# Performance work log

Hardware: AMD Instinct MI355X
Metric: run time of the kernel (lower is better)

## Reference

```python
import jax, jax.numpy as jnp
import numpy as np

N, E, D, HID, OUT, R = 100000, 640000, 128, 128, 128, 8


def setup_inputs() -> dict:
    key = jax.random.key(0)
    ks = jax.random.split(key, 12)
    x = jax.random.normal(ks[0], (N, D), dtype=jnp.float32)
    src = jax.random.randint(ks[1], (E,), 0, N)
    dst = jax.random.randint(ks[2], (E,), 0, N)
    etype = jax.random.randint(ks[3], (E,), 0, R)
    s = 0.05
    W_rel = jax.random.normal(ks[4], (R, D, OUT), dtype=jnp.float32) * s
    loop_w = jax.random.normal(ks[5], (D, OUT), dtype=jnp.float32) * s
    rel_bias = jax.random.normal(ks[6], (OUT,), dtype=jnp.float32) * s
    W1 = jax.random.normal(ks[7], (D + HID, 2 * HID), dtype=jnp.float32) * s
    b1 = jax.random.normal(ks[8], (2 * HID,), dtype=jnp.float32) * s
    W2 = jax.random.normal(ks[9], (D + 2 * HID, OUT), dtype=jnp.float32) * s
    b2 = jax.random.normal(ks[10], (OUT,), dtype=jnp.float32) * s
    return {"x": x, "src": src, "dst": dst, "etype": etype,
            "W_rel": W_rel, "loop_w": loop_w, "rel_bias": rel_bias,
            "W1": W1, "b1": b1, "W2": W2, "b2": b2}


def reference(x, src, dst, etype, W_rel, loop_w, rel_bias, W1, b1, W2, b2):
    n = x.shape[0]
    # RelGraphConv (low_mem): transform all nodes once per relation, then
    # gather the (relation, src)-specific message per edge.  [R, N, OUT]
    h_rel = jnp.einsum('nd,rdo->rno', x, W_rel)
    m = h_rel[etype, src]                                   # [E, OUT]
    agg = jax.ops.segment_sum(m, dst, num_segments=n)       # sum at dst
    msg = agg + x @ loop_w + rel_bias                       # self-loop + bias
    # concat-MLP update (is_block=False -> dst_x = x), activation = tanh
    mid = jnp.tanh(jnp.concatenate([x, msg], axis=1) @ W1 + b1)
    return jnp.concatenate([x, mid], axis=1) @ W2 + b2
```

## Files before the change

kernel.cpp:

```cpp
#include <hip/hip_runtime.h>

#define NN 100000
#define NE 640000
#define RR 8
#define NBIN 800000

typedef unsigned short u16;
typedef u16 u16x4 __attribute__((ext_vector_type(4)));
typedef u16 u16x8 __attribute__((ext_vector_type(8)));
typedef __bf16 bf16x8 __attribute__((ext_vector_type(8)));
typedef float f32x4 __attribute__((ext_vector_type(4)));

#define OFF_MSG     0u
#define OFF_MIDB    51200000u
#define OFF_XB      102400000u
#define OFF_WT      128000000u
#define OFF_W1T     128296960u
#define OFF_W2T     128428032u
#define OFF_BUCKET  128527360u
#define OFF_CSROFF  131088384u
#define OFF_CUR     134289408u
#define OFF_PSUM    137490432u

__device__ inline u16 f2bf(float f) {
  unsigned u = __float_as_uint(f);
  u += 0x7FFF + ((u >> 16) & 1);
  return (u16)(u >> 16);
}
__device__ inline float bf2f(u16 h) { return __uint_as_float(((unsigned)h) << 16); }

__device__ inline int edge_bin(int d, int r) { return d * 8 + r; }

__global__ void k_cvt_x(const float* __restrict__ x, u16* __restrict__ xb) {
  const int i = (blockIdx.x * 256 + threadIdx.x) * 4;
  const float4 v = *(const float4*)(x + i);
  u16x4 o;
  o.x = f2bf(v.x); o.y = f2bf(v.y); o.z = f2bf(v.z); o.w = f2bf(v.w);
  *(u16x4*)(xb + i) = o;
}

__global__ void k_cvt_wrel(const float* __restrict__ W, const float* __restrict__ Lw,
                           u16* __restrict__ Wt) {
  const int idx = blockIdx.x * 256 + threadIdx.x;
  const int r = idx >> 14, o = (idx >> 7) & 127, d = idx & 127;
  Wt[idx] = f2bf(r < 8 ? W[(r << 14) + (d << 7) + o] : Lw[(d << 7) + o]);
}

__global__ void k_cvt_w1(const float* __restrict__ W1, u16* __restrict__ W1t) {
  const int idx = blockIdx.x * 256 + threadIdx.x;
  const int o = idx >> 8, i = idx & 255;
  W1t[idx] = f2bf(W1[i * 256 + o]);
}

__global__ void k_cvt_w2(const float* __restrict__ W2, u16* __restrict__ W2t) {
  const int idx = blockIdx.x * 256 + threadIdx.x;
  const int o = idx / 384, i = idx % 384;
  W2t[idx] = f2bf(W2[i * 128 + o]);
}

__global__ void k_hist(const int* __restrict__ dst, const int* __restrict__ et,
                       int* __restrict__ cnt) {
  const int e = blockIdx.x * 256 + threadIdx.x;
  if (e < NE) atomicAdd(&cnt[edge_bin(dst[e], et[e])], 1);
}

__global__ void k_scanA(const int* __restrict__ cnt, int* __restrict__ psum) {
  __shared__ int sc[256];
  const int tid = threadIdx.x, base = blockIdx.x * 1024 + tid * 4;
  int s = 0;
#pragma unroll
  for (int t = 0; t < 4; ++t) { const int i = base + t; if (i < NBIN) s += cnt[i]; }
  sc[tid] = s; __syncthreads();
  for (int d = 128; d > 0; d >>= 1) {
    if (tid < d) sc[tid] += sc[tid + d];
    __syncthreads();
  }
  if (tid == 0) psum[blockIdx.x] = sc[0];
}

__global__ void k_scanB(int* __restrict__ psum) {
  __shared__ int sc[1024];
  const int tid = threadIdx.x;
  const int v = (tid < 782) ? psum[tid] : 0;
  sc[tid] = v; __syncthreads();
  for (int d = 1; d < 1024; d <<= 1) {
    const int t = (tid >= d) ? sc[tid - d] : 0;
    __syncthreads();
    sc[tid] += t;
    __syncthreads();
  }
  if (tid < 782) psum[tid] = sc[tid] - v;
}

__global__ void k_scanC(int* __restrict__ cnt , const int* __restrict__ psum,
                        int* __restrict__ off) {
  __shared__ int sc[256];
  const int tid = threadIdx.x, base = blockIdx.x * 1024 + tid * 4;
  int c[4], s = 0;
#pragma unroll
  for (int t = 0; t < 4; ++t) {
    const int i = base + t;
    c[t] = (i < NBIN) ? cnt[i] : 0;
    s += c[t];
  }
  sc[tid] = s; __syncthreads();
  for (int d = 1; d < 256; d <<= 1) {
    const int t = (tid >= d) ? sc[tid - d] : 0;
    __syncthreads();
    sc[tid] += t;
    __syncthreads();
  }
  int run = psum[blockIdx.x] + sc[tid] - s;
#pragma unroll
  for (int t = 0; t < 4; ++t) {
    const int i = base + t;
    if (i < NBIN) { off[i] = run; cnt[i] = run; run += c[t]; }
  }
  if (blockIdx.x == 0 && tid == 0) off[NBIN] = NE;
}

__global__ void k_scatter(const int* __restrict__ src, const int* __restrict__ dst,
                          const int* __restrict__ et, int* __restrict__ cur,
                          unsigned* __restrict__ bucket) {
  const int e = blockIdx.x * 256 + threadIdx.x;
  if (e < NE) {
    const int d = dst[e], r = et[e];
    const int pos = atomicAdd(&cur[edge_bin(d, r)], 1);
    bucket[pos] = (unsigned)src[e] | ((unsigned)r << 17);
  }
}

#define ATS 136
#define WCAP 448
__global__ __launch_bounds__(256, 4) void k_edge_msg(
    const u16* __restrict__ xb, const u16* __restrict__ Wt,
    const int* __restrict__ csroff, const unsigned* __restrict__ bucket,
    const float* __restrict__ rel_bias, float* __restrict__ msg) {
  __shared__ u16 At[4 * 32 * ATS];
  __shared__ unsigned wlds[WCAP];
  const int tid = threadIdx.x;
  const int v0 = blockIdx.x * 32;
  const int wave = tid >> 6, lane = tid & 63;
  const int l16 = lane & 15, quad = lane >> 4;
  const int rt = wave & 1, cb = (wave >> 1) << 6;
  const int si = tid >> 3, sj = tid & 7;

  const int gbase = csroff[v0 * 8];
  const int ntot  = csroff[v0 * 8 + 256] - gbase;

  f32x4 acc[4] = {};

  {
    const u16* xp = xb + ((size_t)(v0 + rt * 16 + l16) << 7) + quad * 8;
    bf16x8 afr[4];
#pragma unroll
    for (int t = 0; t < 4; ++t) afr[t] = *(const bf16x8*)(xp + t * 32);
    const u16* wb = Wt + (8 << 14);
#pragma unroll
    for (int c = 0; c < 4; ++c) {
      const u16* wp = wb + (size_t)(cb + c * 16 + l16) * 128 + quad * 8;
#pragma unroll
      for (int t = 0; t < 4; ++t)
        acc[c] = __builtin_amdgcn_mfma_f32_16x16x32_bf16(afr[t], *(const bf16x8*)(wp + t * 32), acc[c], 0, 0, 0);
    }
  }

  {
    const int nst = ntot < WCAP ? ntot : WCAP;
    for (int i = tid; i < nst; i += 256) wlds[i] = bucket[gbase + i];
  }
  __syncthreads();

#pragma unroll
  for (int ph = 0; ph < 2; ++ph) {
    {
      const u16x8 z = {0, 0, 0, 0, 0, 0, 0, 0};
#pragma unroll
      for (int q = 0; q < 4; ++q) {
        u16* dp = &At[q * (32 * ATS) + si * ATS + sj * 16];
        *(u16x8*)dp = z;
        *(u16x8*)(dp + 8) = z;
      }
    }

    {
      const int pbeg = csroff[v0 * 8 + si * 8 + ph * 4] - gbase;
      const int pend = csroff[v0 * 8 + si * 8 + ph * 4 + 4] - gbase;
      const int n = pend - pbeg;
      float a[16] = {};
      int crel = -1;
      unsigned wv[4];
      u16x8 h0[4], h1[4];
#pragma unroll
      for (int j = 0; j < 4; ++j) {
        if (j < n) {
          const int p = pbeg + j;
          const unsigned w = (p < WCAP) ? wlds[p] : bucket[gbase + p];
          wv[j] = w;
          const u16* xp = xb + ((size_t)(w & 0x1FFFFu) << 7) + sj * 16;
          h0[j] = *(const u16x8*)xp;
          h1[j] = *(const u16x8*)(xp + 8);
        }
      }
      for (int ib = 0; ib < n; ib += 4) {
#pragma unroll
        for (int j = 0; j < 4; ++j) {
          const int i = ib + j;
          if (i < n) {
            const int r = (int)((wv[j] >> 17) & 7u);
            if (r != crel) {
              if (crel >= 0) {
                u16x8 o0, o1;
#pragma unroll
                for (int t = 0; t < 8; ++t) { o0[t] = f2bf(a[t]); o1[t] = f2bf(a[8 + t]); }
                u16* dp = &At[(crel & 3) * (32 * ATS) + si * ATS + sj * 16];
                *(u16x8*)dp = o0;
                *(u16x8*)(dp + 8) = o1;
              }
#pragma unroll
              for (int t = 0; t < 16; ++t) a[t] = 0.f;
              crel = r;
            }
#pragma unroll
            for (int t = 0; t < 8; ++t) { a[t] += bf2f(h0[j][t]); a[8 + t] += bf2f(h1[j][t]); }
            const int p = i + 4;
            if (p < n) {
              const int pp = pbeg + p;
              const unsigned w = (pp < WCAP) ? wlds[pp] : bucket[gbase + pp];
              wv[j] = w;
              const u16* xp = xb + ((size_t)(w & 0x1FFFFu) << 7) + sj * 16;
              h0[j] = *(const u16x8*)xp;
              h1[j] = *(const u16x8*)(xp + 8);
            }
          }
        }
      }
      if (crel >= 0) {
        u16x8 o0, o1;
#pragma unroll
        for (int t = 0; t < 8; ++t) { o0[t] = f2bf(a[t]); o1[t] = f2bf(a[8 + t]); }
        u16* dp = &At[(crel & 3) * (32 * ATS) + si * ATS + sj * 16];
        *(u16x8*)dp = o0;
        *(u16x8*)(dp + 8) = o1;
      }
    }
    __syncthreads();

#pragma unroll
    for (int q = 0; q < 4; ++q) {
      bf16x8 afr[4];
#pragma unroll
      for (int t = 0; t < 4; ++t)
        afr[t] = *(const bf16x8*)&At[q * (32 * ATS) + (rt * 16 + l16) * ATS + quad * 8 + t * 32];
      const u16* wb = Wt + ((ph * 4 + q) << 14);
#pragma unroll
      for (int c = 0; c < 4; ++c) {
        const u16* wp = wb + (size_t)(cb + c * 16 + l16) * 128 + quad * 8;
#pragma unroll
        for (int t = 0; t < 4; ++t)
          acc[c] = __builtin_amdgcn_mfma_f32_16x16x32_bf16(afr[t], *(const bf16x8*)(wp + t * 32), acc[c], 0, 0, 0);
      }
    }
    __syncthreads();
  }

#pragma unroll
  for (int c = 0; c < 4; ++c) {
    const int col = cb + c * 16 + l16;
    const float bias = rel_bias[col];
#pragma unroll
    for (int reg = 0; reg < 4; ++reg) {
      const int row = v0 + rt * 16 + quad * 4 + reg;
      msg[(size_t)row * 128 + col] = acc[c][reg] + bias;
    }
  }
}

#define A1S 264
__global__ __launch_bounds__(256) void k_mlp1(
    const u16* __restrict__ xb, const float* __restrict__ msg,
    const u16* __restrict__ W1t, const float* __restrict__ b1,
    u16* __restrict__ midb) {
  __shared__ u16 At[32 * A1S];
  const int tid = threadIdx.x;
  const int v0 = blockIdx.x * 32;
  const int si = tid >> 3, sj = tid & 7;

  {
    const u16* xp = xb + ((size_t)(v0 + si) << 7) + sj * 16;
    *(u16x8*)&At[si * A1S + sj * 16]     = *(const u16x8*)(xp);
    *(u16x8*)&At[si * A1S + sj * 16 + 8] = *(const u16x8*)(xp + 8);
  }
  {
    const float* mp = msg + (size_t)(v0 + si) * 128 + sj * 16;
    u16x8 o0, o1;
#pragma unroll
    for (int t = 0; t < 8; ++t) { o0[t] = f2bf(mp[t]); o1[t] = f2bf(mp[8 + t]); }
    *(u16x8*)&At[si * A1S + 128 + sj * 16]     = o0;
    *(u16x8*)&At[si * A1S + 128 + sj * 16 + 8] = o1;
  }
  __syncthreads();

  const int wave = tid >> 6, lane = tid & 63;
  const int l16 = lane & 15, quad = lane >> 4;
  const int rt = wave & 1, ch = (wave >> 1) << 7;

  f32x4 acc[8] = {};
  for (int kt = 0; kt < 8; ++kt) {
    const bf16x8 af = *(const bf16x8*)&At[(rt * 16 + l16) * A1S + kt * 32 + quad * 8];
#pragma unroll
    for (int ct = 0; ct < 8; ++ct) {
      const u16* wp = W1t + (size_t)(ch + ct * 16 + l16) * 256 + kt * 32 + quad * 8;
      acc[ct] = __builtin_amdgcn_mfma_f32_16x16x32_bf16(af, *(const bf16x8*)(wp), acc[ct], 0, 0, 0);
    }
  }

#pragma unroll
  for (int ct = 0; ct < 8; ++ct) {
    const int col = ch + ct * 16 + l16;
    const float bias = b1[col];
#pragma unroll
    for (int reg = 0; reg < 4; ++reg) {
      const int row = v0 + rt * 16 + quad * 4 + reg;
      midb[(size_t)row * 256 + col] = f2bf(tanhf(acc[ct][reg] + bias));
    }
  }
}

#define A2S 392
__global__ __launch_bounds__(256) void k_mlp2(
    const u16* __restrict__ xb, const u16* __restrict__ midb,
    const u16* __restrict__ W2t, const float* __restrict__ b2,
    float* __restrict__ out) {
  __shared__ u16 At[32 * A2S];
  const int tid = threadIdx.x;
  const int v0 = blockIdx.x * 32;
  const int si = tid >> 3, sj = tid & 7;

  {
    const u16* xp = xb + ((size_t)(v0 + si) << 7) + sj * 16;
    *(u16x8*)&At[si * A2S + sj * 16]     = *(const u16x8*)(xp);
    *(u16x8*)&At[si * A2S + sj * 16 + 8] = *(const u16x8*)(xp + 8);
  }
  {
    const u16* mp = midb + ((size_t)(v0 + si) << 8) + sj * 32;
#pragma unroll
    for (int t = 0; t < 4; ++t)
      *(u16x8*)&At[si * A2S + 128 + sj * 32 + t * 8] = *(const u16x8*)(mp + t * 8);
  }
  __syncthreads();

  const int wave = tid >> 6, lane = tid & 63;
  const int l16 = lane & 15, quad = lane >> 4;
  const int rt = wave & 1, cb = (wave >> 1) << 6;

  f32x4 acc[4] = {};
  for (int kt = 0; kt < 12; ++kt) {
    const bf16x8 af = *(const bf16x8*)&At[(rt * 16 + l16) * A2S + kt * 32 + quad * 8];
#pragma unroll
    for (int ct = 0; ct < 4; ++ct) {
      const u16* wp = W2t + (size_t)(cb + ct * 16 + l16) * 384 + kt * 32 + quad * 8;
      acc[ct] = __builtin_amdgcn_mfma_f32_16x16x32_bf16(af, *(const bf16x8*)(wp), acc[ct], 0, 0, 0);
    }
  }

#pragma unroll
  for (int ct = 0; ct < 4; ++ct) {
    const int col = cb + ct * 16 + l16;
    const float bias = b2[col];
#pragma unroll
    for (int reg = 0; reg < 4; ++reg) {
      const int row = v0 + rt * 16 + quad * 4 + reg;
      out[(size_t)row * 128 + col] = acc[ct][reg] + bias;
    }
  }
}

extern "C" void kernel_launch(void* const* d_in, const int* in_sizes, int n_in,
                              void* d_out, int out_size, void* d_ws, size_t ws_size,
                              hipStream_t stream) {
  (void)in_sizes; (void)n_in; (void)out_size; (void)ws_size;
  const float* x        = (const float*)d_in[0];
  const int*   src      = (const int*)d_in[1];
  const int*   dst      = (const int*)d_in[2];
  const int*   et       = (const int*)d_in[3];
  const float* W_rel    = (const float*)d_in[4];
  const float* loop_w   = (const float*)d_in[5];
  const float* rel_bias = (const float*)d_in[6];
  const float* W1       = (const float*)d_in[7];
  const float* b1       = (const float*)d_in[8];
  const float* W2       = (const float*)d_in[9];
  const float* b2       = (const float*)d_in[10];
  float* out = (float*)d_out;

  char* ws = (char*)d_ws;
  float*    msg    = (float*)(ws + OFF_MSG);
  u16*      midb   = (u16*)(ws + OFF_MIDB);
  u16*      xb     = (u16*)(ws + OFF_XB);
  u16*      Wt     = (u16*)(ws + OFF_WT);
  u16*      W1t    = (u16*)(ws + OFF_W1T);
  u16*      W2t    = (u16*)(ws + OFF_W2T);
  unsigned* bucket = (unsigned*)(ws + OFF_BUCKET);
  int*      csroff = (int*)(ws + OFF_CSROFF);
  int*      cur    = (int*)(ws + OFF_CUR);
  int*      psum   = (int*)(ws + OFF_PSUM);

  hipMemsetAsync(cur, 0, (size_t)NBIN * 4, stream);

  k_cvt_x   <<<(NN * 128) / 1024, 256, 0, stream>>>(x, xb);
  k_cvt_wrel<<<(9 * 16384) / 256, 256, 0, stream>>>(W_rel, loop_w, Wt);
  k_cvt_w1  <<<(256 * 256) / 256, 256, 0, stream>>>(W1, W1t);
  k_cvt_w2  <<<(128 * 384) / 256, 256, 0, stream>>>(W2, W2t);

  k_hist    <<<(NE + 255) / 256, 256, 0, stream>>>(dst, et, cur);
  k_scanA   <<<782, 256, 0, stream>>>(cur, psum);
  k_scanB   <<<1, 1024, 0, stream>>>(psum);
  k_scanC   <<<782, 256, 0, stream>>>(cur, psum, csroff);
  k_scatter <<<(NE + 255) / 256, 256, 0, stream>>>(src, dst, et, cur, bucket);

  k_edge_msg<<<NN / 32, 256, 0, stream>>>(xb, Wt, csroff, bucket, rel_bias, msg);
  k_mlp1    <<<NN / 32, 256, 0, stream>>>(xb, msg, W1t, b1, midb);
  k_mlp2    <<<NN / 32, 256, 0, stream>>>(xb, midb, W2t, b2, out);
}
```

Baseline: 632.7 us.

## Fuse edge aggregation and both MLP layers into one per-tile kernel

Merges the edge-message kernel with the two MLP GEMM kernels so each 32-node tile keeps msg and the tanh hidden layer in shared memory as bf16 instead of writing them to global memory and reading them back. This removes the fp32 msg and bf16 mid round-trips plus two launches. The gather prefetch depth is also raised from 4 to 6 to keep more loads in flight. The cost is higher register pressure and longer per-block work within the existing launch bounds, and the hidden tile (32x264) reuses the edge-stage At buffer, which must be large enough.

```diff
diff --git a/kernel.cpp b/kernel.cpp
--- a/kernel.cpp
+++ b/kernel.cpp
@@ -11,16 +11,14 @@
 typedef __bf16 bf16x8 __attribute__((ext_vector_type(8)));
 typedef float f32x4 __attribute__((ext_vector_type(4)));
 
-#define OFF_MSG     0u
-#define OFF_MIDB    51200000u
-#define OFF_XB      102400000u
-#define OFF_WT      128000000u
-#define OFF_W1T     128296960u
-#define OFF_W2T     128428032u
-#define OFF_BUCKET  128527360u
-#define OFF_CSROFF  131088384u
-#define OFF_CUR     134289408u
-#define OFF_PSUM    137490432u
+#define OFF_XB      0u
+#define OFF_WT      25600000u
+#define OFF_W1T     25894912u
+#define OFF_W2T     26025984u
+#define OFF_BUCKET  26124288u
+#define OFF_CSROFF  28684288u
+#define OFF_CUR     31884292u
+#define OFF_PSUM    35084292u
 
 __device__ inline u16 f2bf(float f) {
   unsigned u = __float_as_uint(f);
@@ -132,10 +130,14 @@
 
 #define ATS 136
 #define WCAP 448
-__global__ __launch_bounds__(256, 4) void k_edge_msg(
+#define PDEP 6
+__global__ __launch_bounds__(256, 4) void k_fused(
     const u16* __restrict__ xb, const u16* __restrict__ Wt,
     const int* __restrict__ csroff, const unsigned* __restrict__ bucket,
-    const float* __restrict__ rel_bias, float* __restrict__ msg) {
+    const float* __restrict__ rel_bias,
+    const u16* __restrict__ W1t, const float* __restrict__ b1,
+    const u16* __restrict__ W2t, const float* __restrict__ b2,
+    float* __restrict__ out) {
   __shared__ u16 At[4 * 32 * ATS];
   __shared__ unsigned wlds[WCAP];
   const int tid = threadIdx.x;
@@ -189,10 +191,10 @@
       const int n = pend - pbeg;
       float a[16] = {};
       int crel = -1;
-      unsigned wv[4];
-      u16x8 h0[4], h1[4];
-#pragma unroll
-      for (int j = 0; j < 4; ++j) {
+      unsigned wv[PDEP];
+      u16x8 h0[PDEP], h1[PDEP];
+#pragma unroll
+      for (int j = 0; j < PDEP; ++j) {
         if (j < n) {
           const int p = pbeg + j;
           const unsigned w = (p < WCAP) ? wlds[p] : bucket[gbase + p];
@@ -202,9 +204,9 @@
           h1[j] = *(const u16x8*)(xp + 8);
         }
       }
-      for (int ib = 0; ib < n; ib += 4) {
-#pragma unroll
-        for (int j = 0; j < 4; ++j) {
+      for (int ib = 0; ib < n; ib += PDEP) {
+#pragma unroll
+        for (int j = 0; j < PDEP; ++j) {
           const int i = ib + j;
           if (i < n) {
             const int r = (int)((wv[j] >> 17) & 7u);
@@ -223,7 +225,7 @@
             }
 #pragma unroll
             for (int t = 0; t < 8; ++t) { a[t] += bf2f(h0[j][t]); a[8 + t] += bf2f(h1[j][t]); }
-            const int p = i + 4;
+            const int p = i + PDEP;
             if (p < n) {
               const int pp = pbeg + p;
               const unsigned w = (pp < WCAP) ? wlds[pp] : bucket[gbase + pp];
@@ -264,114 +266,73 @@
     __syncthreads();
   }
 
+  u16* Mt = At;
+  u16* Ht = At + 32 * 136;
 #pragma unroll
   for (int c = 0; c < 4; ++c) {
     const int col = cb + c * 16 + l16;
     const float bias = rel_bias[col];
 #pragma unroll
     for (int reg = 0; reg < 4; ++reg) {
-      const int row = v0 + rt * 16 + quad * 4 + reg;
-      msg[(size_t)row * 128 + col] = acc[c][reg] + bias;
-    }
-  }
-}
-
-#define A1S 264
-__global__ __launch_bounds__(256) void k_mlp1(
-    const u16* __restrict__ xb, const float* __restrict__ msg,
-    const u16* __restrict__ W1t, const float* __restrict__ b1,
-    u16* __restrict__ midb) {
-  __shared__ u16 At[32 * A1S];
-  const int tid = threadIdx.x;
-  const int v0 = blockIdx.x * 32;
-  const int si = tid >> 3, sj = tid & 7;
+      const int row = rt * 16 + quad * 4 + reg;
+      Mt[row * 136 + col] = f2bf(acc[c][reg] + bias);
+    }
+  }
+  __syncthreads();
 
   {
-    const u16* xp = xb + ((size_t)(v0 + si) << 7) + sj * 16;
-    *(u16x8*)&At[si * A1S + sj * 16]     = *(const u16x8*)(xp);
-    *(u16x8*)&At[si * A1S + sj * 16 + 8] = *(const u16x8*)(xp + 8);
-  }
+    const int ch = (wave >> 1) << 7;
+    f32x4 acc2[8] = {};
+#pragma unroll
+    for (int kt = 0; kt < 8; ++kt) {
+      bf16x8 af;
+      if (kt < 4)
+        af = *(const bf16x8*)(xb + ((size_t)(v0 + rt * 16 + l16) << 7) + kt * 32 + quad * 8);
+      else
+        af = *(const bf16x8*)&Mt[(rt * 16 + l16) * 136 + (kt - 4) * 32 + quad * 8];
+#pragma unroll
+      for (int ct = 0; ct < 8; ++ct) {
+        const u16* wp = W1t + (size_t)(ch + ct * 16 + l16) * 256 + kt * 32 + quad * 8;
+        acc2[ct] = __builtin_amdgcn_mfma_f32_16x16x32_bf16(af, *(const bf16x8*)(wp), acc2[ct], 0, 0, 0);
+      }
+    }
+#pragma unroll
+    for (int ct = 0; ct < 8; ++ct) {
+      const int col = ch + ct * 16 + l16;
+      const float bias = b1[col];
+#pragma unroll
+      for (int reg = 0; reg < 4; ++reg) {
+        const int row = rt * 16 + quad * 4 + reg;
+        Ht[row * 264 + col] = f2bf(tanhf(acc2[ct][reg] + bias));
+      }
+    }
+  }
+  __syncthreads();
+
   {
-    const float* mp = msg + (size_t)(v0 + si) * 128 + sj * 16;
-    u16x8 o0, o1;
-#pragma unroll
-    for (int t = 0; t < 8; ++t) { o0[t] = f2bf(mp[t]); o1[t] = f2bf(mp[8 + t]); }
-    *(u16x8*)&At[si * A1S + 128 + sj * 16]     = o0;
-    *(u16x8*)&At[si * A1S + 128 + sj * 16 + 8] = o1;
-  }
-  __syncthreads();
-
-  const int wave = tid >> 6, lane = tid & 63;
-  const int l16 = lane & 15, quad = lane >> 4;
-  const int rt = wave & 1, ch = (wave >> 1) << 7;
-
-  f32x4 acc[8] = {};
-  for (int kt = 0; kt < 8; ++kt) {
-    const bf16x8 af = *(const bf16x8*)&At[(rt * 16 + l16) * A1S + kt * 32 + quad * 8];
-#pragma unroll
-    for (int ct = 0; ct < 8; ++ct) {
-      const u16* wp = W1t + (size_t)(ch + ct * 16 + l16) * 256 + kt * 32 + quad * 8;
-      acc[ct] = __builtin_amdgcn_mfma_f32_16x16x32_bf16(af, *(const bf16x8*)(wp), acc[ct], 0, 0, 0);
-    }
-  }
-
-#pragma unroll
-  for (int ct = 0; ct < 8; ++ct) {
-    const int col = ch + ct * 16 + l16;
-    const float bias = b1[col];
-#pragma unroll
-    for (int reg = 0; reg < 4; ++reg) {
-      const int row = v0 + rt * 16 + quad * 4 + reg;
-      midb[(size_t)row * 256 + col] = f2bf(tanhf(acc[ct][reg] + bias));
-    }
-  }
-}
-
-#define A2S 392
-__global__ __launch_bounds__(256) void k_mlp2(
-    const u16* __restrict__ xb, const u16* __restrict__ midb,
-    const u16* __restrict__ W2t, const float* __restrict__ b2,
-    float* __restrict__ out) {
-  __shared__ u16 At[32 * A2S];
-  const int tid = threadIdx.x;
-  const int v0 = blockIdx.x * 32;
-  const int si = tid >> 3, sj = tid & 7;
-
-  {
-    const u16* xp = xb + ((size_t)(v0 + si) << 7) + sj * 16;
-    *(u16x8*)&At[si * A2S + sj * 16]     = *(const u16x8*)(xp);
-    *(u16x8*)&At[si * A2S + sj * 16 + 8] = *(const u16x8*)(xp + 8);
-  }
-  {
-    const u16* mp = midb + ((size_t)(v0 + si) << 8) + sj * 32;
-#pragma unroll
-    for (int t = 0; t < 4; ++t)
-      *(u16x8*)&At[si * A2S + 128 + sj * 32 + t * 8] = *(const u16x8*)(mp + t * 8);
-  }
-  __syncthreads();
-
-  const int wave = tid >> 6, lane = tid & 63;
-  const int l16 = lane & 15, quad = lane >> 4;
-  const int rt = wave & 1, cb = (wave >> 1) << 6;
-
-  f32x4 acc[4] = {};
-  for (int kt = 0; kt < 12; ++kt) {
-    const bf16x8 af = *(const bf16x8*)&At[(rt * 16 + l16) * A2S + kt * 32 + quad * 8];
+    f32x4 acc3[4] = {};
+#pragma unroll
+    for (int kt = 0; kt < 12; ++kt) {
+      bf16x8 af;
+      if (kt < 4)
+        af = *(const bf16x8*)(xb + ((size_t)(v0 + rt * 16 + l16) << 7) + kt * 32 + quad * 8);
+      else
+        af = *(const bf16x8*)&Ht[(rt * 16 + l16) * 264 + (kt - 4) * 32 + quad * 8];
+#pragma unroll
+      for (int ct = 0; ct < 4; ++ct) {
+        const u16* wp = W2t + (size_t)(cb + ct * 16 + l16) * 384 + kt * 32 + quad * 8;
+        acc3[ct] = __builtin_amdgcn_mfma_f32_16x16x32_bf16(af, *(const bf16x8*)(wp), acc3[ct], 0, 0, 0);
+      }
+    }
 #pragma unroll
     for (int ct = 0; ct < 4; ++ct) {
-      const u16* wp = W2t + (size_t)(cb + ct * 16 + l16) * 384 + kt * 32 + quad * 8;
-      acc[ct] = __builtin_amdgcn_mfma_f32_16x16x32_bf16(af, *(const bf16x8*)(wp), acc[ct], 0, 0, 0);
-    }
-  }
-
-#pragma unroll
-  for (int ct = 0; ct < 4; ++ct) {
-    const int col = cb + ct * 16 + l16;
-    const float bias = b2[col];
-#pragma unroll
-    for (int reg = 0; reg < 4; ++reg) {
-      const int row = v0 + rt * 16 + quad * 4 + reg;
-      out[(size_t)row * 128 + col] = acc[ct][reg] + bias;
+      const int col = cb + ct * 16 + l16;
+      const float bias = b2[col];
+#pragma unroll
+      for (int reg = 0; reg < 4; ++reg) {
+        const int row = v0 + rt * 16 + quad * 4 + reg;
+        out[(size_t)row * 128 + col] = acc3[ct][reg] + bias;
+      }
     }
   }
 }
@@ -394,8 +355,6 @@
   float* out = (float*)d_out;
 
   char* ws = (char*)d_ws;
-  float*    msg    = (float*)(ws + OFF_MSG);
-  u16*      midb   = (u16*)(ws + OFF_MIDB);
   u16*      xb     = (u16*)(ws + OFF_XB);
   u16*      Wt     = (u16*)(ws + OFF_WT);
   u16*      W1t    = (u16*)(ws + OFF_W1T);
@@ -418,7 +377,6 @@
   k_scanC   <<<782, 256, 0, stream>>>(cur, psum, csroff);
   k_scatter <<<(NE + 255) / 256, 256, 0, stream>>>(src, dst, et, cur, bucket);
 
-  k_edge_msg<<<NN / 32, 256, 0, stream>>>(xb, Wt, csroff, bucket, rel_bias, msg);
-  k_mlp1    <<<NN / 32, 256, 0, stream>>>(xb, msg, W1t, b1, midb);
-  k_mlp2    <<<NN / 32, 256, 0, stream>>>(xb, midb, W2t, b2, out);
-}
+  k_fused   <<<NN / 32, 256, 0, stream>>>(xb, Wt, csroff, bucket, rel_bias,
+                                          W1t, b1, W2t, b2, out);
+}
```

After: 612.8 us. 3.1% less time.
